# Kernel optimization log

Measured on AMD Instinct MI355X. Metric: run time of the kernel, lower is better.

Reference implementation:

```python
import jax, jax.numpy as jnp
import numpy as np
import math

N_HEAD = 16

def setup_inputs() -> dict:
    key = jax.random.key(0)
    k1, k2, k3, k4, k5 = jax.random.split(key, 5)
    B, S, D = 2, 2048, 1024
    return {
        "hidden_states": jax.random.normal(k1, (B, S, D), dtype=jnp.float32),
        "c_attn_w": jax.random.normal(k2, (D, 3 * D), dtype=jnp.float32) * 0.02,
        "c_attn_b": jax.random.normal(k3, (3 * D,), dtype=jnp.float32) * 0.02,
        "c_proj_w": jax.random.normal(k4, (D, D), dtype=jnp.float32) * 0.02,
        "c_proj_b": jax.random.normal(k5, (D,), dtype=jnp.float32) * 0.02,
    }

def reference(hidden_states, c_attn_w, c_attn_b, c_proj_w, c_proj_b):
    B, S, D = hidden_states.shape
    H = N_HEAD
    hd = D // H
    # GPT-2 Conv1D: x @ W + b, W is [in, out]
    qkv = hidden_states @ c_attn_w + c_attn_b            # [B,S,3D]
    q, k, v = jnp.split(qkv, 3, axis=-1)                 # each [B,S,D]
    # sparsify_q/k/v_fn are identity hooks in this config
    def to_heads(x):
        return x.reshape(B, S, H, hd).transpose(0, 2, 1, 3)  # [B,H,S,hd]
    q, k, v = to_heads(q), to_heads(k), to_heads(v)
    scores = jnp.einsum("bhqd,bhkd->bhqk", q, k) / math.sqrt(hd)  # [B,H,S,S]
    causal = jnp.triu(jnp.ones((S, S), dtype=bool), k=1)
    scores = jnp.where(causal, jnp.finfo(scores.dtype).min, scores)
    attn = jax.nn.softmax(scores, axis=-1)
    out = jnp.einsum("bhqk,bhkd->bhqd", attn, v)         # [B,H,S,hd]
    out = out.transpose(0, 2, 1, 3).reshape(B, S, D)
    return out @ c_proj_w + c_proj_b
```

## Files before the change

kernel.cpp:

```cpp
#include <hip/hip_runtime.h>
#include <stdint.h>


#define B_   2
#define S_   2048
#define D_   1024
#define H_   16
#define HD_  64

typedef __bf16 bf16x8 __attribute__((ext_vector_type(8)));
typedef float  f32x4  __attribute__((ext_vector_type(4)));
typedef uint32_t u32x4 __attribute__((ext_vector_type(4)));

__device__ __forceinline__ float b2f(uint16_t u) {
    union { uint32_t i; float f; } x; x.i = ((uint32_t)u) << 16; return x.f;
}
__device__ __forceinline__ uint16_t f2b(float f) {
    uint32_t x = __builtin_bit_cast(uint32_t, f);
    x += 0x7fffu + ((x >> 16) & 1u);
    return (uint16_t)(x >> 16);
}
__device__ __forceinline__ float sq(float f) {
    return fminf(fmaxf(f, -1e4f), 1e4f);
}
__device__ __forceinline__ void async16(const void* g, void* l) {
    __builtin_amdgcn_global_load_lds(
        (const __attribute__((address_space(1))) void*)g,
        (__attribute__((address_space(3))) void*)l, 16, 0, 0);
}

__global__ __launch_bounds__(64)
void kcode(uint16_t* out, float v) { if (threadIdx.x == 0) out[0] = f2b(v); }

__global__ __launch_bounds__(256)
void kconvert(const float* __restrict__ in, uint16_t* __restrict__ out, int n) {
    int i = (blockIdx.x * 256 + threadIdx.x) * 4;
    if (i >= n) return;
    float4 v = *(const float4*)(in + i);
    ushort4 o;
    o.x = f2b(v.x); o.y = f2b(v.y); o.z = f2b(v.z); o.w = f2b(v.w);
    *(ushort4*)(out + i) = o;
}

__global__ __launch_bounds__(256)
void kconvert_bias(const float* __restrict__ ab, const float* __restrict__ pb,
                   uint16_t* __restrict__ bA, uint16_t* __restrict__ bP) {
    int i = (blockIdx.x * 256 + threadIdx.x) * 4;
    const float* src = (i < 3072) ? ab + i : pb + (i - 3072);
    uint16_t*   dst = (i < 3072) ? bA + i : bP + (i - 3072);
    float4 v = *(const float4*)src;
    ushort4 o;
    o.x = f2b(v.x); o.y = f2b(v.y); o.z = f2b(v.z); o.w = f2b(v.w);
    *(ushort4*)dst = o;
}

__global__ __launch_bounds__(256)
void ktranspose_cvt(const float* __restrict__ in, uint16_t* __restrict__ out,
                    int rows, int cols) {
    __shared__ __attribute__((aligned(16))) uint16_t tile[64][68];
    const int tid = threadIdx.x, tx = tid & 15, ty = tid >> 4;
    const int c0 = blockIdx.x * 64, r0 = blockIdx.y * 64;
#pragma unroll
    for (int p = 0; p < 4; ++p) {
        int rr = ty + p * 16;
        float4 v = *(const float4*)(in + (size_t)(r0 + rr) * cols + c0 + tx * 4);
        tile[rr][tx * 4 + 0] = f2b(v.x);
        tile[rr][tx * 4 + 1] = f2b(v.y);
        tile[rr][tx * 4 + 2] = f2b(v.z);
        tile[rr][tx * 4 + 3] = f2b(v.w);
    }
    __syncthreads();
#pragma unroll
    for (int p = 0; p < 4; ++p) {
        int rr = ty + p * 16;
        ushort4 v;
        v.x = tile[tx * 4 + 0][rr];
        v.y = tile[tx * 4 + 1][rr];
        v.z = tile[tx * 4 + 2][rr];
        v.w = tile[tx * 4 + 3][rr];
        *(ushort4*)(out + (size_t)(c0 + rr) * rows + r0 + tx * 4) = v;
    }
}

__global__ __launch_bounds__(256, 2)
void kgemm_qkv(const uint16_t* __restrict__ A, const uint16_t* __restrict__ Bt,
               const uint16_t* __restrict__ bias,
               uint16_t* __restrict__ Qb, uint16_t* __restrict__ Kb,
               uint16_t* __restrict__ Vt) {
    constexpr int KD = 1024;
    __shared__ __attribute__((aligned(16))) uint16_t smem[2 * 128 * 32];
    uint16_t* As = smem;
    uint16_t* Bs = smem + 128 * 32;
    const int tid = threadIdx.x, lane = tid & 63, wid = tid >> 6;
    const int r = lane & 15, qd = lane >> 4;
    const int bm = blockIdx.x * 128, bn = blockIdx.y * 128;
    const int wm = (wid & 1) * 64, wn = (wid >> 1) * 64;
    const int sel = (int)blockIdx.y >> 3;
    f32x4 acc[4][4] = {};

    for (int k0 = 0; k0 < KD; k0 += 32) {
#pragma unroll
        for (int half = 0; half < 2; ++half) {
            int s = half * 256 + tid;
            int row = s >> 2;
            int kq = (s & 3) ^ (row & 3);
            async16(A  + (size_t)(bm + row) * KD + k0 + kq * 8, As + s * 8);
            async16(Bt + (size_t)(bn + row) * KD + k0 + kq * 8, Bs + s * 8);
        }
        __syncthreads();
        bf16x8 af[4], bfr[4];
#pragma unroll
        for (int i = 0; i < 4; ++i) {
            int ra = wm + i * 16 + r;
            af[i]  = *(const bf16x8*)(As + ((ra * 4) + (qd ^ (ra & 3))) * 8);
            int rb = wn + i * 16 + r;
            bfr[i] = *(const bf16x8*)(Bs + ((rb * 4) + (qd ^ (rb & 3))) * 8);
        }
        if (sel != 2) {
#pragma unroll
            for (int i = 0; i < 4; ++i)
#pragma unroll
                for (int j = 0; j < 4; ++j)
                    acc[i][j] = __builtin_amdgcn_mfma_f32_16x16x32_bf16(
                        bfr[j], af[i], acc[i][j], 0, 0, 0);
        } else {
#pragma unroll
            for (int i = 0; i < 4; ++i)
#pragma unroll
                for (int j = 0; j < 4; ++j)
                    acc[i][j] = __builtin_amdgcn_mfma_f32_16x16x32_bf16(
                        af[i], bfr[j], acc[i][j], 0, 0, 0);
        }
        __syncthreads();
    }

    const float SCq = 0.1803368801111204f;
    if (sel != 2) {
        uint16_t* dst = sel ? Kb : Qb;
#pragma unroll
        for (int j = 0; j < 4; ++j) {
            int n0 = bn + wn + j * 16 + qd * 4;
            ushort4 b4 = *(const ushort4*)(bias + n0);
            float bv0 = b2f(b4.x), bv1 = b2f(b4.y),
                  bv2 = b2f(b4.z), bv3 = b2f(b4.w);
            int d = n0 & 1023, h = d >> 6, e0 = d & 63;
#pragma unroll
            for (int i = 0; i < 4; ++i) {
                int m = bm + wm + i * 16 + r;
                int bb = m >> 11, s = m & 2047;
                float v0 = acc[i][j][0] + bv0, v1 = acc[i][j][1] + bv1,
                      v2 = acc[i][j][2] + bv2, v3 = acc[i][j][3] + bv3;
                if (sel == 0) { v0 *= SCq; v1 *= SCq; v2 *= SCq; v3 *= SCq; }
                ushort4 o;
                o.x = f2b(sq(v0)); o.y = f2b(sq(v1));
                o.z = f2b(sq(v2)); o.w = f2b(sq(v3));
                *(ushort4*)(dst + (((size_t)bb * H_ + h) * S_ + s) * HD_ + e0) = o;
            }
        }
    } else {
#pragma unroll
        for (int j = 0; j < 4; ++j) {
            int n = bn + wn + j * 16 + r;
            float bv = b2f(bias[n]);
            int d = n & 1023, h = d >> 6, e = d & 63;
#pragma unroll
            for (int i = 0; i < 4; ++i) {
                int m0 = bm + wm + i * 16 + qd * 4;
                int bb = m0 >> 11, s0 = m0 & 2047;
                ushort4 o;
                o.x = f2b(sq(acc[i][j][0] + bv));
                o.y = f2b(sq(acc[i][j][1] + bv));
                o.z = f2b(sq(acc[i][j][2] + bv));
                o.w = f2b(sq(acc[i][j][3] + bv));
                *(ushort4*)(Vt + (((size_t)bb * H_ + h) * HD_ + e) * S_ + s0) = o;
            }
        }
    }
}

__global__ __launch_bounds__(256, 2)
void kgemm_proj(const uint16_t* __restrict__ A, const uint16_t* __restrict__ Bt,
                const uint16_t* __restrict__ bias, float* __restrict__ out) {
    constexpr int KD = 1024;
    __shared__ __attribute__((aligned(16))) uint16_t smem[2 * 128 * 32];
    uint16_t* As = smem;
    uint16_t* Bs = smem + 128 * 32;
    const int tid = threadIdx.x, lane = tid & 63, wid = tid >> 6;
    const int r = lane & 15, qd = lane >> 4;
    const int bm = blockIdx.x * 128, bn = blockIdx.y * 128;
    const int wm = (wid & 1) * 64, wn = (wid >> 1) * 64;
    f32x4 acc[4][4] = {};

    for (int k0 = 0; k0 < KD; k0 += 32) {
#pragma unroll
        for (int half = 0; half < 2; ++half) {
            int s = half * 256 + tid;
            int row = s >> 2;
            int kq = (s & 3) ^ (row & 3);
            async16(A  + (size_t)(bm + row) * KD + k0 + kq * 8, As + s * 8);
            async16(Bt + (size_t)(bn + row) * KD + k0 + kq * 8, Bs + s * 8);
        }
        __syncthreads();
        bf16x8 af[4], bfr[4];
#pragma unroll
        for (int i = 0; i < 4; ++i) {
            int ra = wm + i * 16 + r;
            af[i]  = *(const bf16x8*)(As + ((ra * 4) + (qd ^ (ra & 3))) * 8);
            int rb = wn + i * 16 + r;
            bfr[i] = *(const bf16x8*)(Bs + ((rb * 4) + (qd ^ (rb & 3))) * 8);
        }
#pragma unroll
        for (int i = 0; i < 4; ++i)
#pragma unroll
            for (int j = 0; j < 4; ++j)
                acc[i][j] = __builtin_amdgcn_mfma_f32_16x16x32_bf16(
                    af[i], bfr[j], acc[i][j], 0, 0, 0);
        __syncthreads();
    }

#pragma unroll
    for (int j = 0; j < 4; ++j) {
        int n = bn + wn + j * 16 + r;
        float bv = b2f(bias[n]);
#pragma unroll
        for (int i = 0; i < 4; ++i) {
            int m0 = bm + wm + i * 16 + qd * 4;
#pragma unroll
            for (int g = 0; g < 4; ++g)
                out[(size_t)(m0 + g) * 1024 + n] = sq(acc[i][j][g] + bv);
        }
    }
}

__global__ __launch_bounds__(256, 2)
void kattn(const uint16_t* __restrict__ Q, const uint16_t* __restrict__ K,
           const uint16_t* __restrict__ Vt, uint16_t* __restrict__ O) {
    const int bh  = blockIdx.y;
    const int tid = threadIdx.x, lane = tid & 63, wid = tid >> 6;
    const int r = lane & 15, qd = lane >> 4;
    const uint16_t* Qb = Q  + (size_t)bh * S_ * HD_;
    const uint16_t* Kb = K  + (size_t)bh * S_ * HD_;
    const uint16_t* Vb = Vt + (size_t)bh * HD_ * S_;
    const int b = bh >> 4, h = bh & 15;

    __shared__ __attribute__((aligned(16))) uint16_t Ks[2][128 * 64];
    __shared__ __attribute__((aligned(16))) uint16_t Vs[2][64 * 128];

    const int qtA = 31 - (int)blockIdx.x;
    const int qtB = (int)blockIdx.x;
    const int Ta = (qtA + 2) >> 1;
    const int Tb = (qtB + 2) >> 1;
    const int T  = Ta + Tb;

    auto stage = [&](int t) {
        const int k0 = (t >= Ta ? t - Ta : t) * 128;
        uint16_t* Kd = Ks[t & 1];
        uint16_t* Vd = Vs[t & 1];
#pragma unroll
        for (int i = 0; i < 4; ++i) {
            int s = i * 256 + tid;
            int row = s >> 3, c = (s & 7) ^ (row & 7);
            async16(Kb + (size_t)(k0 + row) * HD_ + c * 8, Kd + s * 8);
        }
#pragma unroll
        for (int i = 0; i < 4; ++i) {
            int s = i * 256 + tid;
            int row = s >> 4, c = (s & 15) ^ (row & 15);
            async16(Vb + (size_t)row * S_ + k0 + c * 8, Vd + s * 8);
        }
    };

    stage(0);

    const int kswz0 = (qd ^ (r & 7)) * 8;
    const int kswz1 = ((4 + qd) ^ (r & 7)) * 8;

    bf16x8 qf0 = {}, qf1 = {};
    f32x4 oacc[4];
    float lsum = 0.f;
    int q0 = 0, qrow = 0;

#pragma unroll 1
    for (int t = 0; t < T; ++t) {
        const int phase = (t >= Ta) ? 1 : 0;
        const int tloc  = phase ? (t - Ta) : t;
        const int k0    = tloc * 128;
        const int Tph   = phase ? Tb : Ta;
        if (tloc == 0) {
            q0 = (phase ? qtB : qtA) * 64;
            qrow = q0 + wid * 16 + r;
            qf0 = *(const bf16x8*)(Qb + (size_t)qrow * HD_ + qd * 8);
            qf1 = *(const bf16x8*)(Qb + (size_t)qrow * HD_ + 32 + qd * 8);
#pragma unroll
            for (int j = 0; j < 4; ++j)
#pragma unroll
                for (int g = 0; g < 4; ++g) oacc[j][g] = 0.f;
            lsum = 0.f;
        }
        __syncthreads();
        if (t + 1 < T) stage(t + 1);

        const uint16_t* Kc = Ks[t & 1];
        const uint16_t* Vc = Vs[t & 1];

        f32x4 sacc[8] = {};
#pragma unroll
        for (int n = 0; n < 8; ++n) {
            int row = n * 16 + r;
            bf16x8 kf0 = *(const bf16x8*)(Kc + row * 64 + kswz0);
            bf16x8 kf1 = *(const bf16x8*)(Kc + row * 64 + kswz1);
            sacc[n] = __builtin_amdgcn_mfma_f32_16x16x32_bf16(kf0, qf0, sacc[n], 0, 0, 0);
            sacc[n] = __builtin_amdgcn_mfma_f32_16x16x32_bf16(kf1, qf1, sacc[n], 0, 0, 0);
        }
        if (k0 + 127 > q0) {
#pragma unroll
            for (int n = 0; n < 8; ++n) {
                int kvb = k0 + n * 16 + qd * 4;
#pragma unroll
                for (int g = 0; g < 4; ++g)
                    if (kvb + g > qrow) sacc[n][g] = -3e38f;
            }
        }
        uint32_t D0[8], D1[8];
#pragma unroll
        for (int n = 0; n < 8; ++n) {
            float p0 = exp2f(fminf(sacc[n][0], 20.f));
            float p1 = exp2f(fminf(sacc[n][1], 20.f));
            float p2 = exp2f(fminf(sacc[n][2], 20.f));
            float p3 = exp2f(fminf(sacc[n][3], 20.f));
            lsum += (p0 + p1) + (p2 + p3);
            asm("v_cvt_pk_bf16_f32 %0, %1, %2" : "=v"(D0[n]) : "v"(p0), "v"(p1));
            asm("v_cvt_pk_bf16_f32 %0, %1, %2" : "=v"(D1[n]) : "v"(p2), "v"(p3));
        }
#pragma unroll
        for (int m = 0; m < 4; ++m) {
            asm("v_permlane32_swap_b32 %0, %1"
                : "+v"(D0[2 * m]), "+v"(D0[2 * m + 1]));
            asm("v_permlane32_swap_b32 %0, %1"
                : "+v"(D1[2 * m]), "+v"(D1[2 * m + 1]));
            asm("v_permlane16_swap_b32 %0, %1"
                : "+v"(D0[2 * m]), "+v"(D0[2 * m + 1]));
            asm("v_permlane16_swap_b32 %0, %1"
                : "+v"(D1[2 * m]), "+v"(D1[2 * m + 1]));
        }
#pragma unroll
        for (int ks = 0; ks < 4; ++ks) {
            u32x4 w;
            w[0] = D0[2 * ks]; w[1] = D1[2 * ks];
            w[2] = D0[2 * ks + 1]; w[3] = D1[2 * ks + 1];
            bf16x8 pf = __builtin_bit_cast(bf16x8, w);
            int c = ((ks * 4 + qd) ^ r) * 8;
#pragma unroll
            for (int j = 0; j < 4; ++j) {
                bf16x8 vf = *(const bf16x8*)(Vc + (j * 16 + r) * 128 + c);
                oacc[j] = __builtin_amdgcn_mfma_f32_16x16x32_bf16(pf, vf, oacc[j], 0, 0, 0);
            }
        }

        if (tloc == Tph - 1) {
            float ls = lsum;
            ls += __shfl_xor(ls, 16);
            ls += __shfl_xor(ls, 32);
#pragma unroll
            for (int g = 0; g < 4; ++g) {
                float inv = 1.0f / __shfl(ls, qd * 4 + g);
                int rowg = q0 + wid * 16 + qd * 4 + g;
                size_t base = ((size_t)b * S_ + rowg) * D_ + h * HD_;
#pragma unroll
                for (int j = 0; j < 4; ++j)
                    O[base + j * 16 + r] = f2b(sq(oacc[j][g] * inv));
            }
        }
    }
}

extern "C" void kernel_launch(void* const* d_in, const int* in_sizes, int n_in,
                              void* d_out, int out_size, void* d_ws, size_t ws_size,
                              hipStream_t stream) {
    uint16_t* ws = (uint16_t*)d_ws;

    const int exp_sizes[5] = {4194304, 3145728, 3072, 1048576, 1024};
    if (n_in != 5) { kcode<<<1, 64, 0, stream>>>((uint16_t*)d_out, 2950.f); return; }
    for (int i = 0; i < 5; ++i)
        if (in_sizes[i] != exp_sizes[i]) {
            kcode<<<1, 64, 0, stream>>>((uint16_t*)d_out, 3000.f + 100.f * i); return;
        }
    if (out_size != 4194304) { kcode<<<1, 64, 0, stream>>>((uint16_t*)d_out, 2900.f); return; }

    uint16_t* WtA = ws;
    uint16_t* WtP = WtA + 3145728;
    uint16_t* bA  = WtP + 1048576;
    uint16_t* bP  = bA  + 4096;
    uint16_t* Qb  = bP  + 4096;
    uint16_t* Kb  = Qb  + 4194304;
    uint16_t* Vt  = Kb  + 4194304;
    uint16_t* HO  = Vt  + 4194304;
    const size_t NEED = (size_t)((HO + 4194304) - ws) * 2 + 16;
    if (ws_size < NEED) {
        kcode<<<1, 64, 0, stream>>>((uint16_t*)d_out, 1000.f + (float)(ws_size >> 20));
        return;
    }

    kconvert<<<4096, 256, 0, stream>>>((const float*)d_in[0], HO, 4194304);
    kconvert_bias<<<4, 256, 0, stream>>>((const float*)d_in[2], (const float*)d_in[4],
                                         bA, bP);
    ktranspose_cvt<<<dim3(48, 16), 256, 0, stream>>>((const float*)d_in[1], WtA, 1024, 3072);
    ktranspose_cvt<<<dim3(16, 16), 256, 0, stream>>>((const float*)d_in[3], WtP, 1024, 1024);

    kgemm_qkv<<<dim3(32, 24), 256, 0, stream>>>(HO, WtA, bA, Qb, Kb, Vt);
    kattn<<<dim3(16, 32), 256, 0, stream>>>(Qb, Kb, Vt, HO);
    kgemm_proj<<<dim3(32, 8), 256, 0, stream>>>(HO, WtP, bP, (float*)d_out);
}
```

Measured before the change: 205.0 us.

## Restructure attention grid, shrink proj GEMM tile, split QKV loop by output type

The attention kernel no longer pairs a long and a short causal query tile per block. It launches one block per 64-row query tile, ordered longest-first with a head-interleaved mapping, uses 64-key tiles, raises occupancy to 4 blocks per CU, and adds s_setprio around the MFMA sections. The projection GEMM switches to 64x128 tiles to double the block count, and its epilogue is transposed so results are written as vectorised float4 stores. The QKV GEMM moves the sel branch out of the k-loop, so each output path has its own loop. The smaller tiles and extra blocks are meant to improve load balance and CU fill, but they reduce data reuse per block and add more loop iterations.

```diff
diff --git a/kernel.cpp b/kernel.cpp
--- a/kernel.cpp
+++ b/kernel.cpp
@@ -98,7 +98,7 @@
     const int sel = (int)blockIdx.y >> 3;
     f32x4 acc[4][4] = {};
 
-    for (int k0 = 0; k0 < KD; k0 += 32) {
+    auto stage = [&](int k0) {
 #pragma unroll
         for (int half = 0; half < 2; ++half) {
             int s = half * 256 + tid;
@@ -107,35 +107,29 @@
             async16(A  + (size_t)(bm + row) * KD + k0 + kq * 8, As + s * 8);
             async16(Bt + (size_t)(bn + row) * KD + k0 + kq * 8, Bs + s * 8);
         }
-        __syncthreads();
-        bf16x8 af[4], bfr[4];
-#pragma unroll
-        for (int i = 0; i < 4; ++i) {
-            int ra = wm + i * 16 + r;
-            af[i]  = *(const bf16x8*)(As + ((ra * 4) + (qd ^ (ra & 3))) * 8);
-            int rb = wn + i * 16 + r;
-            bfr[i] = *(const bf16x8*)(Bs + ((rb * 4) + (qd ^ (rb & 3))) * 8);
-        }
-        if (sel != 2) {
+    };
+
+    if (sel != 2) {
+        for (int k0 = 0; k0 < KD; k0 += 32) {
+            stage(k0);
+            __syncthreads();
+            bf16x8 af[4], bfr[4];
+#pragma unroll
+            for (int i = 0; i < 4; ++i) {
+                int ra = wm + i * 16 + r;
+                af[i]  = *(const bf16x8*)(As + ((ra * 4) + (qd ^ (ra & 3))) * 8);
+                int rb = wn + i * 16 + r;
+                bfr[i] = *(const bf16x8*)(Bs + ((rb * 4) + (qd ^ (rb & 3))) * 8);
+            }
 #pragma unroll
             for (int i = 0; i < 4; ++i)
 #pragma unroll
                 for (int j = 0; j < 4; ++j)
                     acc[i][j] = __builtin_amdgcn_mfma_f32_16x16x32_bf16(
                         bfr[j], af[i], acc[i][j], 0, 0, 0);
-        } else {
-#pragma unroll
-            for (int i = 0; i < 4; ++i)
-#pragma unroll
-                for (int j = 0; j < 4; ++j)
-                    acc[i][j] = __builtin_amdgcn_mfma_f32_16x16x32_bf16(
-                        af[i], bfr[j], acc[i][j], 0, 0, 0);
-        }
-        __syncthreads();
-    }
-
-    const float SCq = 0.1803368801111204f;
-    if (sel != 2) {
+            __syncthreads();
+        }
+        const float SCq = 0.1803368801111204f;
         uint16_t* dst = sel ? Kb : Qb;
 #pragma unroll
         for (int j = 0; j < 4; ++j) {
@@ -158,6 +152,25 @@
             }
         }
     } else {
+        for (int k0 = 0; k0 < KD; k0 += 32) {
+            stage(k0);
+            __syncthreads();
+            bf16x8 af[4], bfr[4];
+#pragma unroll
+            for (int i = 0; i < 4; ++i) {
+                int ra = wm + i * 16 + r;
+                af[i]  = *(const bf16x8*)(As + ((ra * 4) + (qd ^ (ra & 3))) * 8);
+                int rb = wn + i * 16 + r;
+                bfr[i] = *(const bf16x8*)(Bs + ((rb * 4) + (qd ^ (rb & 3))) * 8);
+            }
+#pragma unroll
+            for (int i = 0; i < 4; ++i)
+#pragma unroll
+                for (int j = 0; j < 4; ++j)
+                    acc[i][j] = __builtin_amdgcn_mfma_f32_16x16x32_bf16(
+                        af[i], bfr[j], acc[i][j], 0, 0, 0);
+            __syncthreads();
+        }
 #pragma unroll
         for (int j = 0; j < 4; ++j) {
             int n = bn + wn + j * 16 + r;
@@ -182,60 +195,73 @@
 void kgemm_proj(const uint16_t* __restrict__ A, const uint16_t* __restrict__ Bt,
                 const uint16_t* __restrict__ bias, float* __restrict__ out) {
     constexpr int KD = 1024;
-    __shared__ __attribute__((aligned(16))) uint16_t smem[2 * 128 * 32];
+    __shared__ __attribute__((aligned(16))) uint16_t smem[(64 + 128) * 32];
     uint16_t* As = smem;
-    uint16_t* Bs = smem + 128 * 32;
+    uint16_t* Bs = smem + 64 * 32;
     const int tid = threadIdx.x, lane = tid & 63, wid = tid >> 6;
     const int r = lane & 15, qd = lane >> 4;
-    const int bm = blockIdx.x * 128, bn = blockIdx.y * 128;
-    const int wm = (wid & 1) * 64, wn = (wid >> 1) * 64;
-    f32x4 acc[4][4] = {};
+    const int bm = blockIdx.x * 64, bn = blockIdx.y * 128;
+    const int wm = (wid & 1) * 32, wn = (wid >> 1) * 64;
+    f32x4 acc[2][4] = {};
 
     for (int k0 = 0; k0 < KD; k0 += 32) {
+        {
+            int s = tid;
+            int row = s >> 2;
+            int kq = (s & 3) ^ (row & 3);
+            async16(A + (size_t)(bm + row) * KD + k0 + kq * 8, As + s * 8);
+        }
 #pragma unroll
         for (int half = 0; half < 2; ++half) {
             int s = half * 256 + tid;
             int row = s >> 2;
             int kq = (s & 3) ^ (row & 3);
-            async16(A  + (size_t)(bm + row) * KD + k0 + kq * 8, As + s * 8);
             async16(Bt + (size_t)(bn + row) * KD + k0 + kq * 8, Bs + s * 8);
         }
         __syncthreads();
-        bf16x8 af[4], bfr[4];
-#pragma unroll
-        for (int i = 0; i < 4; ++i) {
+        bf16x8 af[2], bfr[4];
+#pragma unroll
+        for (int i = 0; i < 2; ++i) {
             int ra = wm + i * 16 + r;
-            af[i]  = *(const bf16x8*)(As + ((ra * 4) + (qd ^ (ra & 3))) * 8);
-            int rb = wn + i * 16 + r;
-            bfr[i] = *(const bf16x8*)(Bs + ((rb * 4) + (qd ^ (rb & 3))) * 8);
-        }
-#pragma unroll
-        for (int i = 0; i < 4; ++i)
+            af[i] = *(const bf16x8*)(As + ((ra * 4) + (qd ^ (ra & 3))) * 8);
+        }
+#pragma unroll
+        for (int j = 0; j < 4; ++j) {
+            int rb = wn + j * 16 + r;
+            bfr[j] = *(const bf16x8*)(Bs + ((rb * 4) + (qd ^ (rb & 3))) * 8);
+        }
+#pragma unroll
+        for (int i = 0; i < 2; ++i)
 #pragma unroll
             for (int j = 0; j < 4; ++j)
                 acc[i][j] = __builtin_amdgcn_mfma_f32_16x16x32_bf16(
-                    af[i], bfr[j], acc[i][j], 0, 0, 0);
+                    bfr[j], af[i], acc[i][j], 0, 0, 0);
         __syncthreads();
     }
 
 #pragma unroll
-    for (int j = 0; j < 4; ++j) {
-        int n = bn + wn + j * 16 + r;
-        float bv = b2f(bias[n]);
-#pragma unroll
-        for (int i = 0; i < 4; ++i) {
-            int m0 = bm + wm + i * 16 + qd * 4;
-#pragma unroll
-            for (int g = 0; g < 4; ++g)
-                out[(size_t)(m0 + g) * 1024 + n] = sq(acc[i][j][g] + bv);
-        }
-    }
-}
-
-__global__ __launch_bounds__(256, 2)
+    for (int i = 0; i < 2; ++i) {
+        int m = bm + wm + i * 16 + r;
+#pragma unroll
+        for (int j = 0; j < 4; ++j) {
+            int n0 = bn + wn + j * 16 + qd * 4;
+            ushort4 b4 = *(const ushort4*)(bias + n0);
+            float4 o;
+            o.x = sq(acc[i][j][0] + b2f(b4.x));
+            o.y = sq(acc[i][j][1] + b2f(b4.y));
+            o.z = sq(acc[i][j][2] + b2f(b4.z));
+            o.w = sq(acc[i][j][3] + b2f(b4.w));
+            *(float4*)(out + (size_t)m * 1024 + n0) = o;
+        }
+    }
+}
+
+__global__ __launch_bounds__(256, 4)
 void kattn(const uint16_t* __restrict__ Q, const uint16_t* __restrict__ K,
            const uint16_t* __restrict__ Vt, uint16_t* __restrict__ O) {
-    const int bh  = blockIdx.y;
+    const int d_  = (int)blockIdx.y * 32 + (int)blockIdx.x;
+    const int bh  = (d_ & 7) + 8 * ((d_ >> 3) & 3);
+    const int qt  = 31 - (d_ >> 5);
     const int tid = threadIdx.x, lane = tid & 63, wid = tid >> 6;
     const int r = lane & 15, qd = lane >> 4;
     const uint16_t* Qb = Q  + (size_t)bh * S_ * HD_;
@@ -243,87 +269,73 @@
     const uint16_t* Vb = Vt + (size_t)bh * HD_ * S_;
     const int b = bh >> 4, h = bh & 15;
 
-    __shared__ __attribute__((aligned(16))) uint16_t Ks[2][128 * 64];
-    __shared__ __attribute__((aligned(16))) uint16_t Vs[2][64 * 128];
-
-    const int qtA = 31 - (int)blockIdx.x;
-    const int qtB = (int)blockIdx.x;
-    const int Ta = (qtA + 2) >> 1;
-    const int Tb = (qtB + 2) >> 1;
-    const int T  = Ta + Tb;
+    __shared__ __attribute__((aligned(16))) uint16_t Ks[2][64 * 64];
+    __shared__ __attribute__((aligned(16))) uint16_t Vs[2][64 * 64];
+
+    const int T = qt + 1;
 
     auto stage = [&](int t) {
-        const int k0 = (t >= Ta ? t - Ta : t) * 128;
+        const int k0 = t * 64;
         uint16_t* Kd = Ks[t & 1];
         uint16_t* Vd = Vs[t & 1];
 #pragma unroll
-        for (int i = 0; i < 4; ++i) {
+        for (int i = 0; i < 2; ++i) {
             int s = i * 256 + tid;
             int row = s >> 3, c = (s & 7) ^ (row & 7);
             async16(Kb + (size_t)(k0 + row) * HD_ + c * 8, Kd + s * 8);
         }
 #pragma unroll
-        for (int i = 0; i < 4; ++i) {
+        for (int i = 0; i < 2; ++i) {
             int s = i * 256 + tid;
-            int row = s >> 4, c = (s & 15) ^ (row & 15);
+            int row = s >> 3, c = (s & 7) ^ (row & 7);
             async16(Vb + (size_t)row * S_ + k0 + c * 8, Vd + s * 8);
         }
     };
 
     stage(0);
+
+    const int q0 = qt * 64;
+    const int qrow = q0 + wid * 16 + r;
+    const bf16x8 qf0 = *(const bf16x8*)(Qb + (size_t)qrow * HD_ + qd * 8);
+    const bf16x8 qf1 = *(const bf16x8*)(Qb + (size_t)qrow * HD_ + 32 + qd * 8);
 
     const int kswz0 = (qd ^ (r & 7)) * 8;
     const int kswz1 = ((4 + qd) ^ (r & 7)) * 8;
 
-    bf16x8 qf0 = {}, qf1 = {};
-    f32x4 oacc[4];
+    f32x4 oacc[4] = {};
     float lsum = 0.f;
-    int q0 = 0, qrow = 0;
 
 #pragma unroll 1
     for (int t = 0; t < T; ++t) {
-        const int phase = (t >= Ta) ? 1 : 0;
-        const int tloc  = phase ? (t - Ta) : t;
-        const int k0    = tloc * 128;
-        const int Tph   = phase ? Tb : Ta;
-        if (tloc == 0) {
-            q0 = (phase ? qtB : qtA) * 64;
-            qrow = q0 + wid * 16 + r;
-            qf0 = *(const bf16x8*)(Qb + (size_t)qrow * HD_ + qd * 8);
-            qf1 = *(const bf16x8*)(Qb + (size_t)qrow * HD_ + 32 + qd * 8);
-#pragma unroll
-            for (int j = 0; j < 4; ++j)
-#pragma unroll
-                for (int g = 0; g < 4; ++g) oacc[j][g] = 0.f;
-            lsum = 0.f;
-        }
         __syncthreads();
         if (t + 1 < T) stage(t + 1);
 
         const uint16_t* Kc = Ks[t & 1];
         const uint16_t* Vc = Vs[t & 1];
 
-        f32x4 sacc[8] = {};
-#pragma unroll
-        for (int n = 0; n < 8; ++n) {
+        f32x4 sacc[4] = {};
+        __builtin_amdgcn_s_setprio(1);
+#pragma unroll
+        for (int n = 0; n < 4; ++n) {
             int row = n * 16 + r;
             bf16x8 kf0 = *(const bf16x8*)(Kc + row * 64 + kswz0);
             bf16x8 kf1 = *(const bf16x8*)(Kc + row * 64 + kswz1);
             sacc[n] = __builtin_amdgcn_mfma_f32_16x16x32_bf16(kf0, qf0, sacc[n], 0, 0, 0);
             sacc[n] = __builtin_amdgcn_mfma_f32_16x16x32_bf16(kf1, qf1, sacc[n], 0, 0, 0);
         }
-        if (k0 + 127 > q0) {
-#pragma unroll
-            for (int n = 0; n < 8; ++n) {
-                int kvb = k0 + n * 16 + qd * 4;
+        __builtin_amdgcn_s_setprio(0);
+        if (t == T - 1) {
+#pragma unroll
+            for (int n = 0; n < 4; ++n) {
+                int kvb = t * 64 + n * 16 + qd * 4;
 #pragma unroll
                 for (int g = 0; g < 4; ++g)
                     if (kvb + g > qrow) sacc[n][g] = -3e38f;
             }
         }
-        uint32_t D0[8], D1[8];
-#pragma unroll
-        for (int n = 0; n < 8; ++n) {
+        uint32_t D0[4], D1[4];
+#pragma unroll
+        for (int n = 0; n < 4; ++n) {
             float p0 = exp2f(fminf(sacc[n][0], 20.f));
             float p1 = exp2f(fminf(sacc[n][1], 20.f));
             float p2 = exp2f(fminf(sacc[n][2], 20.f));
@@ -333,7 +345,7 @@
             asm("v_cvt_pk_bf16_f32 %0, %1, %2" : "=v"(D1[n]) : "v"(p2), "v"(p3));
         }
 #pragma unroll
-        for (int m = 0; m < 4; ++m) {
+        for (int m = 0; m < 2; ++m) {
             asm("v_permlane32_swap_b32 %0, %1"
                 : "+v"(D0[2 * m]), "+v"(D0[2 * m + 1]));
             asm("v_permlane32_swap_b32 %0, %1"
@@ -343,34 +355,34 @@
             asm("v_permlane16_swap_b32 %0, %1"
                 : "+v"(D1[2 * m]), "+v"(D1[2 * m + 1]));
         }
-#pragma unroll
-        for (int ks = 0; ks < 4; ++ks) {
+        __builtin_amdgcn_s_setprio(1);
+#pragma unroll
+        for (int ks = 0; ks < 2; ++ks) {
             u32x4 w;
             w[0] = D0[2 * ks]; w[1] = D1[2 * ks];
             w[2] = D0[2 * ks + 1]; w[3] = D1[2 * ks + 1];
             bf16x8 pf = __builtin_bit_cast(bf16x8, w);
-            int c = ((ks * 4 + qd) ^ r) * 8;
+            int c = ((ks * 4 + qd) ^ (r & 7)) * 8;
 #pragma unroll
             for (int j = 0; j < 4; ++j) {
-                bf16x8 vf = *(const bf16x8*)(Vc + (j * 16 + r) * 128 + c);
+                bf16x8 vf = *(const bf16x8*)(Vc + (j * 16 + r) * 64 + c);
                 oacc[j] = __builtin_amdgcn_mfma_f32_16x16x32_bf16(pf, vf, oacc[j], 0, 0, 0);
             }
         }
-
-        if (tloc == Tph - 1) {
-            float ls = lsum;
-            ls += __shfl_xor(ls, 16);
-            ls += __shfl_xor(ls, 32);
-#pragma unroll
-            for (int g = 0; g < 4; ++g) {
-                float inv = 1.0f / __shfl(ls, qd * 4 + g);
-                int rowg = q0 + wid * 16 + qd * 4 + g;
-                size_t base = ((size_t)b * S_ + rowg) * D_ + h * HD_;
-#pragma unroll
-                for (int j = 0; j < 4; ++j)
-                    O[base + j * 16 + r] = f2b(sq(oacc[j][g] * inv));
-            }
-        }
+        __builtin_amdgcn_s_setprio(0);
+    }
+
+    float ls = lsum;
+    ls += __shfl_xor(ls, 16);
+    ls += __shfl_xor(ls, 32);
+#pragma unroll
+    for (int g = 0; g < 4; ++g) {
+        float inv = 1.0f / __shfl(ls, qd * 4 + g);
+        int rowg = q0 + wid * 16 + qd * 4 + g;
+        size_t base = ((size_t)b * S_ + rowg) * D_ + h * HD_;
+#pragma unroll
+        for (int j = 0; j < 4; ++j)
+            O[base + j * 16 + r] = f2b(sq(oacc[j][g] * inv));
     }
 }
 
@@ -408,6 +420,6 @@
     ktranspose_cvt<<<dim3(16, 16), 256, 0, stream>>>((const float*)d_in[3], WtP, 1024, 1024);
 
     kgemm_qkv<<<dim3(32, 24), 256, 0, stream>>>(HO, WtA, bA, Qb, Kb, Vt);
-    kattn<<<dim3(16, 32), 256, 0, stream>>>(Qb, Kb, Vt, HO);
-    kgemm_proj<<<dim3(32, 8), 256, 0, stream>>>(HO, WtP, bP, (float*)d_out);
-}
+    kattn<<<dim3(32, 32), 256, 0, stream>>>(Qb, Kb, Vt, HO);
+    kgemm_proj<<<dim3(64, 8), 256, 0, stream>>>(HO, WtP, bP, (float*)d_out);
+}
```

Measured after the change: 185.3 us. 9.6% less time.
